# Kernel optimization log

Hardware: AMD Instinct MI355X
Metric: run time of the kernel (lower is better)

## Reference

```python
import jax, jax.numpy as jnp
import numpy as np

VOCAB = 32000
EMB_DIM = 64
BATCH, SEQ = 2, 4096


def setup_inputs() -> dict:
    key = jax.random.key(0)
    kx, kw = jax.random.split(key)
    x = jax.random.normal(kx, (BATCH, SEQ, EMB_DIM), dtype=jnp.float32)
    W = jax.random.normal(kw, (VOCAB, EMB_DIM), dtype=jnp.float32)
    return {"x": x, "W": W}


def reference(x, W):
    # x: [B, S, D] continuous embeddings; W: [V, D] embedding table.
    B, S, D = x.shape
    A = x.reshape(-1, D)                       # [N, D], N = B*S
    # cosine similarity: (A @ W^T) / (|A| |W|)
    nom = A @ W.T                              # [N, V]  (huge intermediate)
    norm_A = jnp.linalg.norm(A, axis=1)        # [N]
    norm_W = jnp.linalg.norm(W, axis=1)        # [V]
    sims = nom / (norm_A[:, None] * norm_W[None, :])
    idx = jnp.argmax(sims, axis=-1)            # [N]
    idx = idx.reshape(B, S)
    onehot = jax.nn.one_hot(idx, W.shape[0], dtype=jnp.float32)  # [B, S, V]
    return onehot
```

## Files before the change

kernel.cpp:

```cpp
#include <hip/hip_runtime.h>

#define VOCAB 32000
#define EMB 64
#define NROWS 8192
#define NCHUNKS 50
#define CCOLS 640
#define CTILES 40
#define NSUB 500
#define SUBPAD 512
#define NZ_BLOCKS 2048
#define PAT 57
#define TOTAL_BLOCKS 3648

typedef __attribute__((ext_vector_type(8))) short bf16x8;
typedef __attribute__((ext_vector_type(4))) float f32x4;
typedef float f4nt __attribute__((ext_vector_type(4)));

__device__ __forceinline__ unsigned enc_f32(float f) {
    unsigned u = __float_as_uint(f);
    return (u & 0x80000000u) ? ~u : (u | 0x80000000u);
}
__device__ __forceinline__ float dec_f32(unsigned e) {
    unsigned u = (e & 0x80000000u) ? (e & 0x7fffffffu) : ~e;
    return __uint_as_float(u);
}
__device__ __forceinline__ unsigned short f2bf(float f) {
    unsigned u = __float_as_uint(f);
    return (unsigned short)((u + 0x7fffu + ((u >> 16) & 1u)) >> 16);
}

__global__ __launch_bounds__(256) void setup_kernel(
    const float* __restrict__ x, const float* __restrict__ W,
    unsigned short* __restrict__ A16, unsigned short* __restrict__ WB16,
    float* __restrict__ invn, float* __restrict__ normA)
{
    int i = blockIdx.x * blockDim.x + threadIdx.x;
    if (i < VOCAB) {
        const float4* w4 = (const float4*)(W + (size_t)i * EMB);
        float4 buf[16];
        float s = 0.f;
        #pragma unroll
        for (int q = 0; q < 16; ++q) {
            float4 w = w4[q]; buf[q] = w;
            s += w.x * w.x + w.y * w.y + w.z * w.z + w.w * w.w;
        }
        float inv = 1.0f / sqrtf(s);
        invn[i] = inv;
        ushort4* dst = (ushort4*)(WB16 + (size_t)i * EMB);
        #pragma unroll
        for (int q = 0; q < 16; ++q) {
            float4 w = buf[q];
            ushort4 u;
            u.x = f2bf(w.x * inv); u.y = f2bf(w.y * inv);
            u.z = f2bf(w.z * inv); u.w = f2bf(w.w * inv);
            dst[q] = u;
        }
    }
    if (i < NROWS) {
        const float4* a4 = (const float4*)(x + (size_t)i * EMB);
        float4 buf[16];
        float s = 0.f;
        #pragma unroll
        for (int q = 0; q < 16; ++q) {
            float4 a = a4[q]; buf[q] = a;
            s += a.x * a.x + a.y * a.y + a.z * a.z + a.w * a.w;
        }
        normA[i] = sqrtf(s);
        ushort4* dst = (ushort4*)(A16 + (size_t)i * EMB);
        #pragma unroll
        for (int q = 0; q < 16; ++q) {
            float4 a = buf[q];
            ushort4 u;
            u.x = f2bf(a.x); u.y = f2bf(a.y); u.z = f2bf(a.z); u.w = f2bf(a.w);
            dst[q] = u;
        }
    }
}

__global__ __launch_bounds__(256) void pass1_kernel(
    const unsigned short* __restrict__ A16,
    const unsigned short* __restrict__ WB16,
    unsigned short* __restrict__ pval, float4* __restrict__ out4)
{
    const int bx = blockIdx.x;
    const int pat = bx / PAT, off = bx - pat * PAT;

    if (off >= 25) {
        const int zid = pat * 32 + (off - 25);
        const f4nt z = {0.f, 0.f, 0.f, 0.f};
        float4* p = out4 + (size_t)zid * 256 + threadIdx.x;
        #pragma unroll 5
        for (int i = 0; i < 125; ++i)
            __builtin_nontemporal_store(z, (f4nt*)(p + (size_t)i * (NZ_BLOCKS * 256)));
        return;
    }

    const int cid = pat * 25 + off;
    const int rowblk = cid & 31, chunk = cid >> 5;
    const int lane = threadIdx.x & 63, wid = threadIdx.x >> 6;
    const int lr = lane & 15, lg = lane >> 4;
    const int m0 = rowblk * 256 + wid * 64;
    const int n0 = chunk * CCOLS;

    bf16x8 a[4][2];
    #pragma unroll
    for (int r = 0; r < 4; ++r)
        #pragma unroll
        for (int kk = 0; kk < 2; ++kk)
            a[r][kk] = *(const bf16x8*)(A16 + (size_t)(m0 + r * 16 + lr) * EMB + kk * 32 + lg * 8);

    float best[4][4];
    #pragma unroll
    for (int r = 0; r < 4; ++r)
        #pragma unroll
        for (int j = 0; j < 4; ++j) best[r][j] = -3e38f;

    const unsigned short* wb = WB16 + (size_t)(n0 + lr) * EMB + lg * 8;
    bf16x8 b0 = *(const bf16x8*)(wb);
    bf16x8 b1 = *(const bf16x8*)(wb + 32);
    for (int t = 0; t < CTILES; ++t) {
        const unsigned short* wn = wb + 16 * EMB;
        bf16x8 nb0 = *(const bf16x8*)(wn);
        bf16x8 nb1 = *(const bf16x8*)(wn + 32);
        #pragma unroll
        for (int r = 0; r < 4; ++r) {
            f32x4 acc = {0.f, 0.f, 0.f, 0.f};
            acc = __builtin_amdgcn_mfma_f32_16x16x32_bf16(a[r][0], b0, acc, 0, 0, 0);
            acc = __builtin_amdgcn_mfma_f32_16x16x32_bf16(a[r][1], b1, acc, 0, 0, 0);
            #pragma unroll
            for (int j = 0; j < 4; ++j) best[r][j] = fmaxf(best[r][j], acc[j]);
        }
        if ((t & 3) == 3) {
            const int sub = chunk * 10 + (t >> 2);
            #pragma unroll
            for (int r = 0; r < 4; ++r)
                #pragma unroll
                for (int j = 0; j < 4; ++j) {
                    float v = best[r][j];
                    v = fmaxf(v, __shfl_xor(v, 1));
                    v = fmaxf(v, __shfl_xor(v, 2));
                    v = fmaxf(v, __shfl_xor(v, 4));
                    v = fmaxf(v, __shfl_xor(v, 8));
                    if (lr == 0)
                        pval[(size_t)(m0 + r * 16 + lg * 4 + j) * SUBPAD + sub] =
                            (unsigned short)(enc_f32(v) >> 16);
                    best[r][j] = -3e38f;
                }
        }
        b0 = nb0; b1 = nb1;
        wb = wn;
    }
}

__global__ __launch_bounds__(64) void finalize_kernel(
    const float* __restrict__ x, const float* __restrict__ W,
    const float* __restrict__ invn, const unsigned short* __restrict__ pval,
    const float* __restrict__ normA, float* __restrict__ out)
{
    const int row = blockIdx.x;
    const int lane = threadIdx.x;
    __shared__ float xs[EMB];
    xs[lane] = x[(size_t)row * EMB + lane];

    const unsigned short* pr = pval + (size_t)row * SUBPAD + lane * 8;
    ushort4 v0 = *(const ushort4*)(pr);
    ushort4 v1 = *(const ushort4*)(pr + 4);
    unsigned short vals[8] = {v0.x, v0.y, v0.z, v0.w, v1.x, v1.y, v1.z, v1.w};

    unsigned mx = 0;
    #pragma unroll
    for (int k = 0; k < 8; ++k)
        if (lane * 8 + k < NSUB) mx = mx > (unsigned)vals[k] ? mx : (unsigned)vals[k];
    #pragma unroll
    for (int off = 1; off < 64; off <<= 1) {
        unsigned o = __shfl_xor(mx, off);
        mx = mx > o ? mx : o;
    }
    float thr = dec_f32(mx << 16) - 0.009f * normA[row];
    unsigned thr_enc = enc_f32(thr);

    __syncthreads();
    const float4* xs4 = (const float4*)xs;
    unsigned long long best = 0ull;

    #pragma unroll
    for (int k = 0; k < 8; ++k) {
        int sub = lane * 8 + k;
        bool c = (sub < NSUB) && ((((unsigned)vals[k] + 1u) << 16) > thr_enc);
        unsigned long long m = __ballot(c);
        while (m) {
            int src = __ffsll((long long)m) - 1;
            m &= m - 1;
            unsigned v = ((unsigned)(src * 8 + k)) * 64u + (unsigned)lane;
            const float4* w4 = (const float4*)(W + (size_t)v * EMB);
            float p0 = 0.f, p1 = 0.f, p2 = 0.f, p3 = 0.f;
            #pragma unroll
            for (int q = 0; q < 16; ++q) {
                float4 aa = xs4[q]; float4 ww = w4[q];
                p0 = fmaf(aa.x, ww.x, p0);
                p1 = fmaf(aa.y, ww.y, p1);
                p2 = fmaf(aa.z, ww.z, p2);
                p3 = fmaf(aa.w, ww.w, p3);
            }
            float s = ((p0 + p1) + (p2 + p3)) * invn[v];
            unsigned long long kk =
                ((unsigned long long)enc_f32(s) << 32) | (unsigned)(~v);
            best = best > kk ? best : kk;
        }
    }
    #pragma unroll
    for (int off = 1; off < 64; off <<= 1) {
        unsigned long long o = __shfl_xor(best, off);
        best = best > o ? best : o;
    }
    if (lane == 0)
        out[(size_t)row * VOCAB + (size_t)(unsigned)(~(unsigned)best)] = 1.0f;
}

extern "C" void kernel_launch(void* const* d_in, const int* in_sizes, int n_in,
                              void* d_out, int out_size, void* d_ws, size_t ws_size,
                              hipStream_t stream) {
    const float* x = (const float*)d_in[0];
    const float* W = (const float*)d_in[1];
    float* out = (float*)d_out;

    char* ws = (char*)d_ws;
    unsigned short* WB16 = (unsigned short*)(ws);
    unsigned short* A16  = (unsigned short*)(ws + 4096000);
    float* invn          = (float*)(ws + 5144576);
    float* normA         = (float*)(ws + 5272576);
    unsigned short* pval = (unsigned short*)(ws + 5305344);

    setup_kernel<<<dim3((VOCAB + 255) / 256), dim3(256), 0, stream>>>(
        x, W, A16, WB16, invn, normA);

    pass1_kernel<<<dim3(TOTAL_BLOCKS), dim3(256), 0, stream>>>(
        A16, WB16, pval, (float4*)out);

    finalize_kernel<<<dim3(NROWS), dim3(64), 0, stream>>>(
        x, W, invn, pval, normA, out);
}
```

Before: 262.3 us.

## Split output zeroing across setup and pass1, use fewer larger compute blocks

Moves part of the output zero-fill into the setup kernel so the memset overlaps the normalization and bf16 conversion work. The pass1 kernel now runs 320 compute blocks, each scanning 3200 vocab columns instead of 640, interleaved one in twelve among zero-fill blocks that cover the rest of the output with a grid-stride loop. The aim is to hide the bandwidth-bound one-hot zeroing behind compute and cut per-block reload overhead. Fewer compute blocks lowers MFMA parallelism, so the longer per-block scans could become the critical path.

```diff
diff --git a/kernel.cpp b/kernel.cpp
--- a/kernel.cpp
+++ b/kernel.cpp
@@ -3,14 +3,17 @@
 #define VOCAB 32000
 #define EMB 64
 #define NROWS 8192
-#define NCHUNKS 50
-#define CCOLS 640
-#define CTILES 40
 #define NSUB 500
 #define SUBPAD 512
-#define NZ_BLOCKS 2048
-#define PAT 57
-#define TOTAL_BLOCKS 3648
+#define NCOMPUTE 320
+#define K2_BLOCKS 4096
+#define NZ2 (K2_BLOCKS - NCOMPUTE)
+#define K1_SETUP 125
+#define K1_ZERO 875
+#define K1_ITERS 28
+#define K1_F4 (K1_ZERO * 256 * K1_ITERS)
+#define TOTAL_F4 (NROWS * (VOCAB / 4))
+#define K2_F4 (TOTAL_F4 - K1_F4)
 
 typedef __attribute__((ext_vector_type(8))) short bf16x8;
 typedef __attribute__((ext_vector_type(4))) float f32x4;
@@ -29,12 +32,23 @@
     return (unsigned short)((u + 0x7fffu + ((u >> 16) & 1u)) >> 16);
 }
 
-__global__ __launch_bounds__(256) void setup_kernel(
+__global__ __launch_bounds__(256) void k1_kernel(
     const float* __restrict__ x, const float* __restrict__ W,
     unsigned short* __restrict__ A16, unsigned short* __restrict__ WB16,
-    float* __restrict__ invn, float* __restrict__ normA)
+    float* __restrict__ invn, float* __restrict__ normA,
+    float4* __restrict__ out4)
 {
-    int i = blockIdx.x * blockDim.x + threadIdx.x;
+    const int bx = blockIdx.x;
+    if (bx >= K1_SETUP) {
+        const int zid = bx - K1_SETUP;
+        const f4nt z = {0.f, 0.f, 0.f, 0.f};
+        float4* p = out4 + (size_t)zid * 256 + threadIdx.x;
+        #pragma unroll 4
+        for (int j = 0; j < K1_ITERS; ++j)
+            __builtin_nontemporal_store(z, (f4nt*)(p + (size_t)j * (K1_ZERO * 256)));
+        return;
+    }
+    int i = bx * 256 + threadIdx.x;
     if (i < VOCAB) {
         const float4* w4 = (const float4*)(W + (size_t)i * EMB);
         float4 buf[16];
@@ -77,30 +91,32 @@
     }
 }
 
-__global__ __launch_bounds__(256) void pass1_kernel(
+__global__ __launch_bounds__(256) void k2_kernel(
     const unsigned short* __restrict__ A16,
     const unsigned short* __restrict__ WB16,
     unsigned short* __restrict__ pval, float4* __restrict__ out4)
 {
     const int bx = blockIdx.x;
-    const int pat = bx / PAT, off = bx - pat * PAT;
-
-    if (off >= 25) {
-        const int zid = pat * 32 + (off - 25);
+    const bool is_compute = (bx % 12 == 0) && (bx / 12 < NCOMPUTE);
+
+    if (!is_compute) {
+        const int nc = min(NCOMPUTE, (bx + 11) / 12);
+        const int zid = bx - nc;
         const f4nt z = {0.f, 0.f, 0.f, 0.f};
-        float4* p = out4 + (size_t)zid * 256 + threadIdx.x;
-        #pragma unroll 5
-        for (int i = 0; i < 125; ++i)
-            __builtin_nontemporal_store(z, (f4nt*)(p + (size_t)i * (NZ_BLOCKS * 256)));
+        float4* base = out4 + K1_F4;
+        unsigned i = (unsigned)zid * 256u + threadIdx.x;
+        const unsigned stride = (unsigned)NZ2 * 256u;
+        for (; i < (unsigned)K2_F4; i += stride)
+            __builtin_nontemporal_store(z, (f4nt*)(base + i));
         return;
     }
 
-    const int cid = pat * 25 + off;
-    const int rowblk = cid & 31, chunk = cid >> 5;
+    const int cid = bx / 12;
+    const int rowblk = cid & 31, cg = cid >> 5;
     const int lane = threadIdx.x & 63, wid = threadIdx.x >> 6;
     const int lr = lane & 15, lg = lane >> 4;
     const int m0 = rowblk * 256 + wid * 64;
-    const int n0 = chunk * CCOLS;
+    const int n0 = cg * 3200;
 
     bf16x8 a[4][2];
     #pragma unroll
@@ -118,7 +134,7 @@
     const unsigned short* wb = WB16 + (size_t)(n0 + lr) * EMB + lg * 8;
     bf16x8 b0 = *(const bf16x8*)(wb);
     bf16x8 b1 = *(const bf16x8*)(wb + 32);
-    for (int t = 0; t < CTILES; ++t) {
+    for (int t = 0; t < 200; ++t) {
         const unsigned short* wn = wb + 16 * EMB;
         bf16x8 nb0 = *(const bf16x8*)(wn);
         bf16x8 nb1 = *(const bf16x8*)(wn + 32);
@@ -131,7 +147,7 @@
             for (int j = 0; j < 4; ++j) best[r][j] = fmaxf(best[r][j], acc[j]);
         }
         if ((t & 3) == 3) {
-            const int sub = chunk * 10 + (t >> 2);
+            const int sub = cg * 50 + (t >> 2);
             #pragma unroll
             for (int r = 0; r < 4; ++r)
                 #pragma unroll
@@ -231,10 +247,10 @@
     float* normA         = (float*)(ws + 5272576);
     unsigned short* pval = (unsigned short*)(ws + 5305344);
 
-    setup_kernel<<<dim3((VOCAB + 255) / 256), dim3(256), 0, stream>>>(
-        x, W, A16, WB16, invn, normA);
-
-    pass1_kernel<<<dim3(TOTAL_BLOCKS), dim3(256), 0, stream>>>(
+    k1_kernel<<<dim3(K1_SETUP + K1_ZERO), dim3(256), 0, stream>>>(
+        x, W, A16, WB16, invn, normA, (float4*)out);
+
+    k2_kernel<<<dim3(K2_BLOCKS), dim3(256), 0, stream>>>(
         A16, WB16, pval, (float4*)out);
 
     finalize_kernel<<<dim3(NROWS), dim3(64), 0, stream>>>(
```

Result: slower. 513.6 us (+95.8%).

## Fuse setup into pass1: convert and normalize W/x to bf16 in-register

Applied to the files above, without the earlier changes.

Removes the separate setup kernel. The main kernel now loads fp32 W and x directly, computes the row norms with cross-lane shuffles, converts to bf16 in registers and double-buffers the W loads across groups. The finalize kernel recomputes the norms of x and W inline instead of reading precomputed arrays. The zero-fill blocks are regridded to 4096 blocks using a grid-stride loop. This saves one launch and the round trip of the bf16 copies, but every column block now re-reads fp32 W (twice the bytes) and redoes the norm math per row block.

```diff
diff --git a/kernel.cpp b/kernel.cpp
--- a/kernel.cpp
+++ b/kernel.cpp
@@ -3,14 +3,13 @@
 #define VOCAB 32000
 #define EMB 64
 #define NROWS 8192
-#define NCHUNKS 50
-#define CCOLS 640
-#define CTILES 40
 #define NSUB 500
 #define SUBPAD 512
-#define NZ_BLOCKS 2048
-#define PAT 57
-#define TOTAL_BLOCKS 3648
+#define NCOMP 1600
+#define NZERO 4096
+#define PAT 89
+#define TOTAL_BLOCKS 5696
+#define TOTAL_F4 (NROWS * (VOCAB / 4))
 
 typedef __attribute__((ext_vector_type(8))) short bf16x8;
 typedef __attribute__((ext_vector_type(4))) float f32x4;
@@ -28,70 +27,91 @@
     unsigned u = __float_as_uint(f);
     return (unsigned short)((u + 0x7fffu + ((u >> 16) & 1u)) >> 16);
 }
-
-__global__ __launch_bounds__(256) void setup_kernel(
+__device__ __forceinline__ bf16x8 packbf(float4 a, float4 b, float inv) {
+    bf16x8 r;
+    r[0] = (short)f2bf(a.x * inv); r[1] = (short)f2bf(a.y * inv);
+    r[2] = (short)f2bf(a.z * inv); r[3] = (short)f2bf(a.w * inv);
+    r[4] = (short)f2bf(b.x * inv); r[5] = (short)f2bf(b.y * inv);
+    r[6] = (short)f2bf(b.z * inv); r[7] = (short)f2bf(b.w * inv);
+    return r;
+}
+
+#define LOADB(buf, g)                                                        \
+    {                                                                        \
+        _Pragma("unroll")                                                    \
+        for (int tt = 0; tt < 4; ++tt) {                                     \
+            const float4* wr = (const float4*)(W + (size_t)(n0 + (g) * 64 +  \
+                                   tt * 16 + lr) * EMB) + lg * 2;            \
+            buf[tt][0] = wr[0];                                              \
+            buf[tt][1] = wr[1];                                              \
+            buf[tt][2] = wr[8];                                              \
+            buf[tt][3] = wr[9];                                              \
+        }                                                                    \
+    }
+
+#define STORE_SUB(sub)                                                       \
+    {                                                                        \
+        _Pragma("unroll")                                                    \
+        for (int r = 0; r < 4; ++r) {                                        \
+            _Pragma("unroll")                                                \
+            for (int j = 0; j < 4; ++j) {                                    \
+                float v = best[r][j];                                        \
+                v = fmaxf(v, __shfl_xor(v, 1));                              \
+                v = fmaxf(v, __shfl_xor(v, 2));                              \
+                v = fmaxf(v, __shfl_xor(v, 4));                              \
+                v = fmaxf(v, __shfl_xor(v, 8));                              \
+                if (lr == 0)                                                 \
+                    pval[(size_t)(m0 + r * 16 + lg * 4 + j) * SUBPAD +       \
+                         (sub)] = (unsigned short)(enc_f32(v) >> 16);        \
+                best[r][j] = -3e38f;                                         \
+            }                                                                \
+        }                                                                    \
+    }
+
+#define PROCESS(buf, sub)                                                    \
+    {                                                                        \
+        _Pragma("unroll")                                                    \
+        for (int tt = 0; tt < 4; ++tt) {                                     \
+            float4 w0 = buf[tt][0], w1 = buf[tt][1];                         \
+            float4 w2 = buf[tt][2], w3 = buf[tt][3];                         \
+            float p = w0.x * w0.x + w0.y * w0.y + w0.z * w0.z + w0.w * w0.w; \
+            p += w1.x * w1.x + w1.y * w1.y + w1.z * w1.z + w1.w * w1.w;      \
+            p += w2.x * w2.x + w2.y * w2.y + w2.z * w2.z + w2.w * w2.w;      \
+            p += w3.x * w3.x + w3.y * w3.y + w3.z * w3.z + w3.w * w3.w;      \
+            p += __shfl_xor(p, 16);                                          \
+            p += __shfl_xor(p, 32);                                          \
+            float inv = 1.0f / sqrtf(p);                                     \
+            bf16x8 b0 = packbf(w0, w1, inv);                                 \
+            bf16x8 b1 = packbf(w2, w3, inv);                                 \
+            _Pragma("unroll")                                                \
+            for (int r = 0; r < 4; ++r) {                                    \
+                f32x4 acc = {0.f, 0.f, 0.f, 0.f};                            \
+                acc = __builtin_amdgcn_mfma_f32_16x16x32_bf16(               \
+                    a[r][0], b0, acc, 0, 0, 0);                              \
+                acc = __builtin_amdgcn_mfma_f32_16x16x32_bf16(               \
+                    a[r][1], b1, acc, 0, 0, 0);                              \
+                _Pragma("unroll")                                            \
+                for (int j = 0; j < 4; ++j)                                  \
+                    best[r][j] = fmaxf(best[r][j], acc[j]);                  \
+            }                                                                \
+        }                                                                    \
+        STORE_SUB(sub)                                                       \
+    }
+
+__global__ __launch_bounds__(256) void mega_kernel(
     const float* __restrict__ x, const float* __restrict__ W,
-    unsigned short* __restrict__ A16, unsigned short* __restrict__ WB16,
-    float* __restrict__ invn, float* __restrict__ normA)
-{
-    int i = blockIdx.x * blockDim.x + threadIdx.x;
-    if (i < VOCAB) {
-        const float4* w4 = (const float4*)(W + (size_t)i * EMB);
-        float4 buf[16];
-        float s = 0.f;
-        #pragma unroll
-        for (int q = 0; q < 16; ++q) {
-            float4 w = w4[q]; buf[q] = w;
-            s += w.x * w.x + w.y * w.y + w.z * w.z + w.w * w.w;
-        }
-        float inv = 1.0f / sqrtf(s);
-        invn[i] = inv;
-        ushort4* dst = (ushort4*)(WB16 + (size_t)i * EMB);
-        #pragma unroll
-        for (int q = 0; q < 16; ++q) {
-            float4 w = buf[q];
-            ushort4 u;
-            u.x = f2bf(w.x * inv); u.y = f2bf(w.y * inv);
-            u.z = f2bf(w.z * inv); u.w = f2bf(w.w * inv);
-            dst[q] = u;
-        }
-    }
-    if (i < NROWS) {
-        const float4* a4 = (const float4*)(x + (size_t)i * EMB);
-        float4 buf[16];
-        float s = 0.f;
-        #pragma unroll
-        for (int q = 0; q < 16; ++q) {
-            float4 a = a4[q]; buf[q] = a;
-            s += a.x * a.x + a.y * a.y + a.z * a.z + a.w * a.w;
-        }
-        normA[i] = sqrtf(s);
-        ushort4* dst = (ushort4*)(A16 + (size_t)i * EMB);
-        #pragma unroll
-        for (int q = 0; q < 16; ++q) {
-            float4 a = buf[q];
-            ushort4 u;
-            u.x = f2bf(a.x); u.y = f2bf(a.y); u.z = f2bf(a.z); u.w = f2bf(a.w);
-            dst[q] = u;
-        }
-    }
-}
-
-__global__ __launch_bounds__(256) void pass1_kernel(
-    const unsigned short* __restrict__ A16,
-    const unsigned short* __restrict__ WB16,
     unsigned short* __restrict__ pval, float4* __restrict__ out4)
 {
     const int bx = blockIdx.x;
     const int pat = bx / PAT, off = bx - pat * PAT;
 
     if (off >= 25) {
-        const int zid = pat * 32 + (off - 25);
+        const int zid = pat * 64 + (off - 25);
         const f4nt z = {0.f, 0.f, 0.f, 0.f};
-        float4* p = out4 + (size_t)zid * 256 + threadIdx.x;
-        #pragma unroll 5
-        for (int i = 0; i < 125; ++i)
-            __builtin_nontemporal_store(z, (f4nt*)(p + (size_t)i * (NZ_BLOCKS * 256)));
+        unsigned i = (unsigned)zid * 256u + threadIdx.x;
+        const unsigned stride = (unsigned)NZERO * 256u;
+        for (; i < (unsigned)TOTAL_F4; i += stride)
+            __builtin_nontemporal_store(z, (f4nt*)(out4 + i));
         return;
     }
 
@@ -100,14 +120,15 @@
     const int lane = threadIdx.x & 63, wid = threadIdx.x >> 6;
     const int lr = lane & 15, lg = lane >> 4;
     const int m0 = rowblk * 256 + wid * 64;
-    const int n0 = chunk * CCOLS;
+    const int n0 = chunk * 640;
 
     bf16x8 a[4][2];
     #pragma unroll
-    for (int r = 0; r < 4; ++r)
-        #pragma unroll
-        for (int kk = 0; kk < 2; ++kk)
-            a[r][kk] = *(const bf16x8*)(A16 + (size_t)(m0 + r * 16 + lr) * EMB + kk * 32 + lg * 8);
+    for (int r = 0; r < 4; ++r) {
+        const float4* xr = (const float4*)(x + (size_t)(m0 + r * 16 + lr) * EMB) + lg * 2;
+        a[r][0] = packbf(xr[0], xr[1], 1.0f);
+        a[r][1] = packbf(xr[8], xr[9], 1.0f);
+    }
 
     float best[4][4];
     #pragma unroll
@@ -115,52 +136,29 @@
         #pragma unroll
         for (int j = 0; j < 4; ++j) best[r][j] = -3e38f;
 
-    const unsigned short* wb = WB16 + (size_t)(n0 + lr) * EMB + lg * 8;
-    bf16x8 b0 = *(const bf16x8*)(wb);
-    bf16x8 b1 = *(const bf16x8*)(wb + 32);
-    for (int t = 0; t < CTILES; ++t) {
-        const unsigned short* wn = wb + 16 * EMB;
-        bf16x8 nb0 = *(const bf16x8*)(wn);
-        bf16x8 nb1 = *(const bf16x8*)(wn + 32);
-        #pragma unroll
-        for (int r = 0; r < 4; ++r) {
-            f32x4 acc = {0.f, 0.f, 0.f, 0.f};
-            acc = __builtin_amdgcn_mfma_f32_16x16x32_bf16(a[r][0], b0, acc, 0, 0, 0);
-            acc = __builtin_amdgcn_mfma_f32_16x16x32_bf16(a[r][1], b1, acc, 0, 0, 0);
-            #pragma unroll
-            for (int j = 0; j < 4; ++j) best[r][j] = fmaxf(best[r][j], acc[j]);
-        }
-        if ((t & 3) == 3) {
-            const int sub = chunk * 10 + (t >> 2);
-            #pragma unroll
-            for (int r = 0; r < 4; ++r)
-                #pragma unroll
-                for (int j = 0; j < 4; ++j) {
-                    float v = best[r][j];
-                    v = fmaxf(v, __shfl_xor(v, 1));
-                    v = fmaxf(v, __shfl_xor(v, 2));
-                    v = fmaxf(v, __shfl_xor(v, 4));
-                    v = fmaxf(v, __shfl_xor(v, 8));
-                    if (lr == 0)
-                        pval[(size_t)(m0 + r * 16 + lg * 4 + j) * SUBPAD + sub] =
-                            (unsigned short)(enc_f32(v) >> 16);
-                    best[r][j] = -3e38f;
-                }
-        }
-        b0 = nb0; b1 = nb1;
-        wb = wn;
+    float4 ra[4][4], rb[4][4];
+    LOADB(ra, 0);
+    #pragma unroll
+    for (int gp = 0; gp < 5; ++gp) {
+        LOADB(rb, gp * 2 + 1);
+        PROCESS(ra, chunk * 10 + gp * 2);
+        if (gp < 4) LOADB(ra, gp * 2 + 2);
+        PROCESS(rb, chunk * 10 + gp * 2 + 1);
     }
 }
 
 __global__ __launch_bounds__(64) void finalize_kernel(
     const float* __restrict__ x, const float* __restrict__ W,
-    const float* __restrict__ invn, const unsigned short* __restrict__ pval,
-    const float* __restrict__ normA, float* __restrict__ out)
+    const unsigned short* __restrict__ pval, float* __restrict__ out)
 {
     const int row = blockIdx.x;
     const int lane = threadIdx.x;
     __shared__ float xs[EMB];
-    xs[lane] = x[(size_t)row * EMB + lane];
+    float e = x[(size_t)row * EMB + lane];
+    xs[lane] = e;
+    float nsq = e * e;
+    #pragma unroll
+    for (int off = 1; off < 64; off <<= 1) nsq += __shfl_xor(nsq, off);
 
     const unsigned short* pr = pval + (size_t)row * SUBPAD + lane * 8;
     ushort4 v0 = *(const ushort4*)(pr);
@@ -176,7 +174,7 @@
         unsigned o = __shfl_xor(mx, off);
         mx = mx > o ? mx : o;
     }
-    float thr = dec_f32(mx << 16) - 0.009f * normA[row];
+    float thr = dec_f32(mx << 16) - 0.009f * sqrtf(nsq);
     unsigned thr_enc = enc_f32(thr);
 
     __syncthreads();
@@ -194,15 +192,17 @@
             unsigned v = ((unsigned)(src * 8 + k)) * 64u + (unsigned)lane;
             const float4* w4 = (const float4*)(W + (size_t)v * EMB);
             float p0 = 0.f, p1 = 0.f, p2 = 0.f, p3 = 0.f;
+            float wsq = 0.f;
             #pragma unroll
             for (int q = 0; q < 16; ++q) {
                 float4 aa = xs4[q]; float4 ww = w4[q];
+                wsq += ww.x * ww.x + ww.y * ww.y + ww.z * ww.z + ww.w * ww.w;
                 p0 = fmaf(aa.x, ww.x, p0);
                 p1 = fmaf(aa.y, ww.y, p1);
                 p2 = fmaf(aa.z, ww.z, p2);
                 p3 = fmaf(aa.w, ww.w, p3);
             }
-            float s = ((p0 + p1) + (p2 + p3)) * invn[v];
+            float s = ((p0 + p1) + (p2 + p3)) * (1.0f / sqrtf(wsq));
             unsigned long long kk =
                 ((unsigned long long)enc_f32(s) << 32) | (unsigned)(~v);
             best = best > kk ? best : kk;
@@ -224,19 +224,11 @@
     const float* W = (const float*)d_in[1];
     float* out = (float*)d_out;
 
-    char* ws = (char*)d_ws;
-    unsigned short* WB16 = (unsigned short*)(ws);
-    unsigned short* A16  = (unsigned short*)(ws + 4096000);
-    float* invn          = (float*)(ws + 5144576);
-    float* normA         = (float*)(ws + 5272576);
-    unsigned short* pval = (unsigned short*)(ws + 5305344);
-
-    setup_kernel<<<dim3((VOCAB + 255) / 256), dim3(256), 0, stream>>>(
-        x, W, A16, WB16, invn, normA);
-
-    pass1_kernel<<<dim3(TOTAL_BLOCKS), dim3(256), 0, stream>>>(
-        A16, WB16, pval, (float4*)out);
+    unsigned short* pval = (unsigned short*)d_ws;
+
+    mega_kernel<<<dim3(TOTAL_BLOCKS), dim3(256), 0, stream>>>(
+        x, W, pval, (float4*)out);
 
     finalize_kernel<<<dim3(NROWS), dim3(64), 0, stream>>>(
-        x, W, invn, pval, normA, out);
-}
+        x, W, pval, out);
+}
```

Result: slower. 349.3 us (+33.2%).
